# Performance work log

Measured on AMD Instinct MI355X. Metric: run time of the kernel, lower is better.

The kernel has to match this reference:

```python
import jax, jax.numpy as jnp
import numpy as np

BETA = 0.9       # leak factor (snn.Leaky beta)
THRESH = 1.0     # default snn.Leaky threshold
ALPHA = 2.0      # default ATan surrogate alpha

@jax.custom_vjp
def atan_spike(x):
    # Heaviside forward, ATan surrogate backward (snntorch default spike_grad)
    return (x > 0).astype(x.dtype)

def _atan_fwd(x):
    return (x > 0).astype(x.dtype), x

def _atan_bwd(x, g):
    # d/dx ~ (alpha/2) / (1 + (pi/2 * alpha * x)^2)
    return (g * (ALPHA / 2) / (1 + (jnp.pi / 2 * ALPHA * x) ** 2),)

atan_spike.defvjp(_atan_fwd, _atan_bwd)

def setup_inputs() -> dict:
    key = jax.random.key(0)
    k1, k2 = jax.random.split(key)
    B, IN, OUT, T = 64, 1024, 1024, 256
    x = jax.random.normal(k1, (B, IN, T), dtype=jnp.float32)
    W = jax.random.normal(k2, (OUT, IN), dtype=jnp.float32) * (1.0 / np.sqrt(IN))
    return {"x": x, "W": W}

def reference(x, W):
    # Batch all per-timestep GEMMs into one contraction: syn[b,o,t]
    syn = jnp.einsum('bit,oi->bot', x, W)
    syn_t = jnp.moveaxis(syn, -1, 0)  # [T, B, OUT]
    mem0 = jnp.zeros(syn.shape[:-1], syn.dtype)  # [B, OUT]

    def step(mem, s):
        # snntorch Leaky (subtract reset): reset from previous mem (detached),
        # then state update, then spike from new mem.
        reset = jax.lax.stop_gradient((mem > THRESH).astype(mem.dtype))
        mem = BETA * mem + s - reset * THRESH
        spk = atan_spike(mem - THRESH)
        return mem, spk

    _, spks = jax.lax.scan(step, mem0, syn_t)  # spks: [T, B, OUT]
    return jnp.moveaxis(spks, 0, -1)  # [B, OUT, T]
```

## Files before the change

kernel.cpp:

```cpp
#include <hip/hip_runtime.h>


#define B_DIM 64
#define IN_DIM 1024
#define OUT_DIM 1024
#define T_DIM 256

typedef int v4i __attribute__((ext_vector_type(4)));
typedef int v16i __attribute__((ext_vector_type(16)));
typedef double v4d __attribute__((ext_vector_type(4)));

#define LO_OFF   0ull
#define WSL_OFF  67108864ull
#define XSL_OFF  73400320ull
#define AL_OFF   174063616ull
#define BE_OFF   174067712ull
#define PART_OFF 174133248ull
#define WS_NEED  175181824ull

__device__ __forceinline__ void gload_lds16(const void* g, void* l)
{
    __builtin_amdgcn_global_load_lds(
        (const __attribute__((address_space(1))) void*)g,
        (__attribute__((address_space(3))) void*)l, 16, 0, 0);
}

__device__ __forceinline__ void dig4_extract(unsigned bits, int bem,
                                             signed char* d )
{
    const int be = (bits >> 23) & 255;
    unsigned M = (bits & 0x7fffffu) | (be ? 0x800000u : 0u);
    const int sh = be - bem + 4;
    unsigned fix = 0;
    if (sh >= 0) fix = M << sh;
    else if (sh > -32) fix = M >> (-sh);
    int d0 = (fix >> 21) & 127, d1 = (fix >> 14) & 127,
        d2 = (fix >> 7) & 127,  d3 = fix & 127;
    if (bits & 0x80000000u) { d0 = -d0; d1 = -d1; d2 = -d2; d3 = -d3; }
    d[0] = (signed char)d0; d[1] = (signed char)d1;
    d[2] = (signed char)d2; d[3] = (signed char)d3;
}

__global__ __launch_bounds__(256) void k_beta_part(const float* __restrict__ x,
                                                   float* __restrict__ part)
{
    const int ic = blockIdx.x;
    const int b  = blockIdx.y;
    const int t  = threadIdx.x;
    const float* p = x + ((size_t)b * IN_DIM + ic * 64) * T_DIM + t;
    float m = 0.f;
    #pragma unroll 4
    for (int i = 0; i < 64; ++i) m = fmaxf(m, fabsf(p[(size_t)i * T_DIM]));
    part[((size_t)b * 16 + ic) * T_DIM + t] = m;
}

__global__ __launch_bounds__(256) void k_beta(const float* __restrict__ part,
                                              int* __restrict__ beta_e)
{
    const int b = blockIdx.x, t = threadIdx.x;
    float m = 0.f;
    #pragma unroll
    for (int ic = 0; ic < 16; ++ic)
        m = fmaxf(m, part[((size_t)b * 16 + ic) * T_DIM + t]);
    int e = 0;
    if (m > 0.f) frexpf(m, &e);
    beta_e[b * T_DIM + t] = e;
}

__global__ __launch_bounds__(256) void k_slice_x(const float* __restrict__ x,
    const int* __restrict__ beta_e, signed char* __restrict__ xsl)
{
    __shared__ float ft[64][65];
    const int tb = blockIdx.x;
    const int ib = blockIdx.y;
    const int b  = blockIdx.z;
    const int tid = threadIdx.x;
    const int t0 = tb * 64, i0 = ib * 64;
    #pragma unroll
    for (int p = 0; p < 16; ++p) {
        int id = tid + p * 256;
        int il = id >> 6, tl = id & 63;
        ft[il][tl] = x[((size_t)b * IN_DIM + i0 + il) * T_DIM + t0 + tl];
    }
    __syncthreads();

    const int t32l = tid >> 7;
    const int ksl  = (tid >> 6) & 1;
    const int lane = tid & 63;
    const int t_local = t32l * 32 + (lane & 31);
    const int k_local = ksl * 32 + (lane >> 5) * 16;
    const int e = beta_e[b * T_DIM + t0 + t_local];
    const int bem = e + 126;

    signed char dig[16][4];
    #pragma unroll
    for (int j = 0; j < 16; ++j)
        dig4_extract(__float_as_uint(ft[k_local + j][t_local]), bem, dig[j]);

    #pragma unroll
    for (int p = 0; p < 4; ++p) {
        int w[4];
        #pragma unroll
        for (int g = 0; g < 4; ++g)
            w[g] = (dig[4*g][p] & 0xff) | ((dig[4*g+1][p] & 0xff) << 8) |
                   ((dig[4*g+2][p] & 0xff) << 16) | ((dig[4*g+3][p] & 0xff) << 24);
        const size_t base =
            ((((size_t)p * B_DIM + b) * 8 + (tb * 2 + t32l)) * 32 + (ib * 2 + ksl)) * 1024
            + lane * 16;
        *(v4i*)&xsl[base] = (v4i){w[0], w[1], w[2], w[3]};
    }
}

__global__ __launch_bounds__(256) void k_slice_w(const float* __restrict__ W,
    signed char* __restrict__ wsl, int* __restrict__ alpha_e)
{
    __shared__ float red[256];
    __shared__ float wrow[1024];
    __shared__ int se;
    const int o = blockIdx.x, tid = threadIdx.x;
    float4 v = *(const float4*)&W[(size_t)o * IN_DIM + tid * 4];
    *(float4*)&wrow[tid * 4] = v;
    float m = fmaxf(fmaxf(fabsf(v.x), fabsf(v.y)), fmaxf(fabsf(v.z), fabsf(v.w)));
    red[tid] = m; __syncthreads();
    for (int s = 128; s > 0; s >>= 1) {
        if (tid < s) red[tid] = fmaxf(red[tid], red[tid + s]);
        __syncthreads();
    }
    if (tid == 0) { int e = 0; if (red[0] > 0.f) frexpf(red[0], &e); se = e; alpha_e[o] = e; }
    __syncthreads();
    if (tid >= 64) return;
    const int bem = se + 126;
    const int ks = tid >> 1, khalf = tid & 1;
    const int k0 = tid * 16;
    const int lane = (o & 31) + 32 * khalf;

    signed char dig[16][4];
    #pragma unroll
    for (int j = 0; j < 16; ++j)
        dig4_extract(__float_as_uint(wrow[k0 + j]), bem, dig[j]);

    #pragma unroll
    for (int p = 0; p < 4; ++p) {
        int w[4];
        #pragma unroll
        for (int g = 0; g < 4; ++g)
            w[g] = (dig[4*g][p] & 0xff) | ((dig[4*g+1][p] & 0xff) << 8) |
                   ((dig[4*g+2][p] & 0xff) << 16) | ((dig[4*g+3][p] & 0xff) << 24);
        const size_t base =
            (((size_t)p * 32 + (o >> 5)) * 32 + ks) * 1024 + lane * 16;
        *(v4i*)&wsl[base] = (v4i){w[0], w[1], w[2], w[3]};
    }
}

#define OZ_LOADS(PF)                                                        \
    {                                                                       \
        _Pragma("unroll")                                                   \
        for (int j = 0; j < 4; ++j) {                                       \
            gload_lds16(gp[j], &LB[PF][lbase + j * 8192]);                  \
            gp[j] += 1024;                                                  \
        }                                                                   \
    }

#define OZ_MATH(CUR)                                                        \
    {                                                                       \
        const signed char* base_ = LB[CUR];                                 \
        v4i af[4];                                                          \
        _Pragma("unroll")                                                   \
        for (int p = 0; p < 4; ++p)                                         \
            af[p] = *(const v4i*)(base_ + p * 4096 + aoffm);                \
        __builtin_amdgcn_s_setprio(1);                                      \
        _Pragma("unroll")                                                   \
        for (int q = 0; q < 4; ++q) {                                       \
            v4i b0 = *(const v4i*)(base_ + 16384 + q * 4096 + boffm);       \
            v4i b1 = *(const v4i*)(base_ + 16384 + q * 4096 + boffm + 1024);\
            _Pragma("unroll")                                               \
            for (int p = 0; p + q < 4; ++p) {                               \
                accA[p + q] = __builtin_amdgcn_mfma_i32_32x32x32_i8(        \
                    af[p], b0, accA[p + q], 0, 0, 0);                       \
                accB[p + q] = __builtin_amdgcn_mfma_i32_32x32x32_i8(        \
                    af[p], b1, accB[p + q], 0, 0, 0);                       \
            }                                                               \
        }                                                                   \
        __builtin_amdgcn_s_setprio(0);                                      \
    }

#define VMBAR(N)                                                            \
    do {                                                                    \
        asm volatile("s_waitcnt vmcnt(" #N ")" ::: "memory");               \
        __builtin_amdgcn_s_barrier();                                       \
    } while (0)

__global__ __launch_bounds__(512, 2) void k_oz_gemm(
    const signed char* __restrict__ wsl, const signed char* __restrict__ xsl,
    const int* __restrict__ alpha_e, const int* __restrict__ beta_e,
    float* __restrict__ syn_hi, float* __restrict__ syn_lo)
{
    __shared__ __align__(16) signed char LB[3][32768];

    const int tid = threadIdx.x;
    const int lane = tid & 63, wave = tid >> 6;
    const int tb = blockIdx.x;
    const int ob = blockIdx.y;
    const int b  = blockIdx.z;
    const int o0 = ob * 128, t0 = tb * 128;
    const int woh = wave >> 1;
    const int wth = wave & 1;
    const int l16 = lane * 16;

    v16i accA[4], accB[4];
    #pragma unroll
    for (int s = 0; s < 4; ++s) {
        accA[s] = (v16i){0,0,0,0,0,0,0,0,0,0,0,0,0,0,0,0};
        accB[s] = (v16i){0,0,0,0,0,0,0,0,0,0,0,0,0,0,0,0};
    }

    const signed char* gp[4];
    #pragma unroll
    for (int j = 0; j < 4; ++j) {
        const int s = 8 * j + wave;
        if (s < 16) {
            gp[j] = wsl + ((size_t)(s >> 2) << 20)
                        + ((size_t)(4 * ob + (s & 3)) << 15) + l16;
        } else {
            const int t = s - 16;
            gp[j] = xsl + ((size_t)(t >> 2) << 24) + ((size_t)b << 18)
                        + ((size_t)(4 * tb + (t & 3)) << 15) + l16;
        }
    }
    const int lbase = wave * 1024;

    const int aoffm = woh * 1024 + l16;
    const int boffm = wth * 2048 + l16;

    OZ_LOADS(0)
    OZ_LOADS(1)
    VMBAR(4);

    #pragma unroll 1
    for (int it = 0; it < 10; ++it) {
        OZ_LOADS(2) OZ_MATH(0) VMBAR(4);
        OZ_LOADS(0) OZ_MATH(1) VMBAR(4);
        OZ_LOADS(1) OZ_MATH(2) VMBAR(4);
    }
    OZ_MATH(0) VMBAR(0);
    OZ_MATH(1)

    const int lr = lane & 31;
    const int rv = (lr + 1) * 0x01010101;
    const v4i pav  = {rv, rv, rv, rv};
    const v4i onev = {0x01010101, 0x01010101, 0x01010101, 0x01010101};
    const v16i z = (v16i){0,0,0,0,0,0,0,0,0,0,0,0,0,0,0,0};
    v16i d1 = __builtin_amdgcn_mfma_i32_32x32x32_i8(pav, onev, z, 0, 0, 0);
    v16i d2 = __builtin_amdgcn_mfma_i32_32x32x32_i8(onev, pav, z, 0, 0, 0);

    const int col = (d2[0] >> 5) - 1;
    const int gtA = t0 + wth * 64 + col;
    const int gtB = gtA + 32;
    const int ebA = beta_e[b * T_DIM + gtA];
    const int ebB = beta_e[b * T_DIM + gtB];
    float* ohiA = syn_hi + ((size_t)b * OUT_DIM + o0) * T_DIM + gtA;
    float* oloA = syn_lo + ((size_t)b * OUT_DIM + o0) * T_DIM + gtA;

    const double C0 = 0x1p-14, C1 = 0x1p-21, C2 = 0x1p-28, C3 = 0x1p-35;
    #pragma unroll
    for (int r = 0; r < 16; ++r) {
        const int row = (d1[r] >> 5) - 1;
        const int go = woh * 32 + row;
        const int ea = alpha_e[o0 + go];
        double vA = (double)accA[0][r] * C0 + (double)accA[1][r] * C1 +
                    (double)accA[2][r] * C2 + (double)accA[3][r] * C3;
        double vB = (double)accB[0][r] * C0 + (double)accB[1][r] * C1 +
                    (double)accB[2][r] * C2 + (double)accB[3][r] * C3;
        double synA = ldexp(vA, ea + ebA);
        double synB = ldexp(vB, ea + ebB);
        float hiA = (float)synA;
        float loA = (float)(synA - (double)hiA);
        float hiB = (float)synB;
        float loB = (float)(synB - (double)hiB);
        const size_t off = (size_t)go * T_DIM;
        ohiA[off] = hiA;       oloA[off] = loA;
        ohiA[off + 32] = hiB;  oloA[off + 32] = loB;
    }
}

#define BM 128
#define BN 128
#define BK 16
#define LDA 130

__global__ __launch_bounds__(256, 2) void spk_gemm_mfma64p_kernel(
    const float* __restrict__ x, const float* __restrict__ W,
    float* __restrict__ syn_hi, float* __restrict__ syn_lo)
{
    const int tid  = threadIdx.x;
    const int lane = tid & 63;
    const int wave = tid >> 6;
    const int tb = blockIdx.x, ob = blockIdx.y, b = blockIdx.z;

    __shared__ __align__(16) double As[BK][LDA];
    __shared__ __align__(16) double Bs[BK][LDA];

    const v4d zz = {0.0, 0.0, 0.0, 0.0};
    v4d d1 = __builtin_amdgcn_mfma_f64_16x16x4f64((double)lane, 1.0, zz, 0, 0, 0);
    v4d d2 = __builtin_amdgcn_mfma_f64_16x16x4f64(1.0, (double)lane, zz, 0, 0, 0);
    const bool a_h1 = (((int)d1[0] & 3) == 0);
    const bool b_h1 = (((int)d2[0] & 3) == 0);
    int drow[4];
    #pragma unroll
    for (int r = 0; r < 4; ++r) {
        const int v = (int)d1[r];
        drow[r] = (a_h1 ? (v - 96) >> 2 : (v - 6) >> 4) & 15;
    }
    const int am = a_h1 ? (lane & 15) : (lane >> 2);
    const int ak = a_h1 ? (lane >> 4) : (lane & 3);
    const int bn = b_h1 ? (lane & 15) : (lane >> 2);
    const int bk = b_h1 ? (lane >> 4) : (lane & 3);
    const int dcol = lane & 15;

    const int o0 = ob * BM, t0 = tb * BN;
    const float* Wp = W + (size_t)o0 * IN_DIM;
    const float* xp = x + (size_t)b * IN_DIM * T_DIM + t0;
    const int wo = (wave >> 1) * 64, wt = (wave & 1) * 64;

    v4d acc[4][4];
    #pragma unroll
    for (int i = 0; i < 4; ++i)
        #pragma unroll
        for (int j = 0; j < 4; ++j) acc[i][j] = zz;

    const int ar0 = tid / 4, ac = (tid % 4) * 4;
    const int bkr0 = tid / 32, btc = (tid % 32) * 4;

    float4 pa[2], pb[2];
    #pragma unroll
    for (int p = 0; p < 2; ++p) {
        pa[p] = *(const float4*)&Wp[(size_t)(ar0 + p * 64) * IN_DIM + ac];
        pb[p] = *(const float4*)&xp[(size_t)(bkr0 + p * 8) * T_DIM + btc];
    }

    for (int k0 = 0; k0 < IN_DIM; k0 += BK) {
        #pragma unroll
        for (int p = 0; p < 2; ++p) {
            const int r = ar0 + p * 64;
            As[ac + 0][r] = (double)pa[p].x; As[ac + 1][r] = (double)pa[p].y;
            As[ac + 2][r] = (double)pa[p].z; As[ac + 3][r] = (double)pa[p].w;
            const int kr = bkr0 + p * 8;
            Bs[kr][btc + 0] = (double)pb[p].x; Bs[kr][btc + 1] = (double)pb[p].y;
            Bs[kr][btc + 2] = (double)pb[p].z; Bs[kr][btc + 3] = (double)pb[p].w;
        }
        if (k0 + BK < IN_DIM) {
            #pragma unroll
            for (int p = 0; p < 2; ++p) {
                pa[p] = *(const float4*)&Wp[(size_t)(ar0 + p * 64) * IN_DIM + k0 + BK + ac];
                pb[p] = *(const float4*)&xp[(size_t)(bkr0 + p * 8 + k0 + BK) * T_DIM + btc];
            }
        }
        __syncthreads();
        #pragma unroll
        for (int kk = 0; kk < 4; ++kk) {
            const int kra = kk * 4 + ak, krb = kk * 4 + bk;
            double a[4], bb[4];
            #pragma unroll
            for (int i = 0; i < 4; ++i) a[i] = As[kra][wo + i * 16 + am];
            #pragma unroll
            for (int j = 0; j < 4; ++j) bb[j] = Bs[krb][wt + j * 16 + bn];
            #pragma unroll
            for (int i = 0; i < 4; ++i)
                #pragma unroll
                for (int j = 0; j < 4; ++j)
                    acc[i][j] = __builtin_amdgcn_mfma_f64_16x16x4f64(a[i], bb[j], acc[i][j], 0, 0, 0);
        }
        __syncthreads();
    }

    float* ohi = syn_hi + ((size_t)b * OUT_DIM + o0) * T_DIM + t0;
    float* olo = syn_lo + ((size_t)b * OUT_DIM + o0) * T_DIM + t0;
    #pragma unroll
    for (int i = 0; i < 4; ++i)
        #pragma unroll
        for (int j = 0; j < 4; ++j) {
            const int col = wt + j * 16 + dcol;
            #pragma unroll
            for (int r = 0; r < 4; ++r) {
                double s = acc[i][j][r];
                float hi = (float)s;
                float lo = (float)(s - (double)hi);
                const size_t off = (size_t)(wo + i * 16 + drow[r]) * T_DIM + col;
                ohi[off] = hi; olo[off] = lo;
            }
        }
}

__global__ __launch_bounds__(256) void spk_scan_f64_kernel(
    float* __restrict__ hi, const float* __restrict__ lo)
{
    const int TC = 16;
    __shared__ float thi[256][TC + 1];
    __shared__ float tlo[256][TC + 1];
    const int tid = threadIdx.x;
    const size_t row0 = (size_t)blockIdx.x * 256;

    double mem = 0.0;
    for (int t0 = 0; t0 < T_DIM; t0 += TC) {
        #pragma unroll
        for (int p = 0; p < 4; ++p) {
            int id = tid + p * 256;
            int r = id / 4, c = (id % 4) * 4;
            size_t g = (row0 + r) * T_DIM + t0 + c;
            float4 vh = *(const float4*)&hi[g];
            thi[r][c] = vh.x; thi[r][c+1] = vh.y; thi[r][c+2] = vh.z; thi[r][c+3] = vh.w;
            float4 vl = *(const float4*)&lo[g];
            tlo[r][c] = vl.x; tlo[r][c+1] = vl.y; tlo[r][c+2] = vl.z; tlo[r][c+3] = vl.w;
        }
        __syncthreads();
        float spk[TC];
        #pragma unroll
        for (int t = 0; t < TC; ++t) {
            double s = (double)thi[tid][t] + (double)tlo[tid][t];
            double reset = (mem > 1.0) ? 1.0 : 0.0;
            mem = 0.9 * mem + s - reset;
            spk[t] = ((mem - 1.0) > 0.0) ? 1.0f : 0.0f;
        }
        __syncthreads();
        #pragma unroll
        for (int t = 0; t < TC; ++t) thi[tid][t] = spk[t];
        __syncthreads();
        #pragma unroll
        for (int p = 0; p < 4; ++p) {
            int id = tid + p * 256;
            int r = id / 4, c = (id % 4) * 4;
            float4 v = make_float4(thi[r][c], thi[r][c+1], thi[r][c+2], thi[r][c+3]);
            *(float4*)&hi[(row0 + r) * T_DIM + t0 + c] = v;
        }
        __syncthreads();
    }
}

extern "C" void kernel_launch(void* const* d_in, const int* in_sizes, int n_in,
                              void* d_out, int out_size, void* d_ws, size_t ws_size,
                              hipStream_t stream)
{
    const float* x = (const float*)d_in[0];
    const float* W = (const float*)d_in[1];
    float* hi = (float*)d_out;
    char* ws = (char*)d_ws;
    float* lo = (float*)(ws + LO_OFF);

    if (ws_size >= WS_NEED) {
        signed char* wsl = (signed char*)(ws + WSL_OFF);
        signed char* xsl = (signed char*)(ws + XSL_OFF);
        int* alpha = (int*)(ws + AL_OFF);
        int* beta  = (int*)(ws + BE_OFF);
        float* part = (float*)(ws + PART_OFF);

        k_beta_part<<<dim3(16, B_DIM), dim3(256), 0, stream>>>(x, part);
        k_beta<<<dim3(B_DIM), dim3(256), 0, stream>>>(part, beta);
        k_slice_w<<<dim3(OUT_DIM), dim3(256), 0, stream>>>(W, wsl, alpha);
        k_slice_x<<<dim3(4, 16, B_DIM), dim3(256), 0, stream>>>(x, beta, xsl);
        k_oz_gemm<<<dim3(2, 8, B_DIM), dim3(512), 0, stream>>>(wsl, xsl, alpha, beta, hi, lo);
    } else {
        spk_gemm_mfma64p_kernel<<<dim3(2, 8, B_DIM), dim3(256), 0, stream>>>(x, W, hi, lo);
    }
    spk_scan_f64_kernel<<<dim3((B_DIM * OUT_DIM) / 256), dim3(256), 0, stream>>>(hi, lo);
}
```

Measured before the change: 348.4 us.

## Fuse LIF scan into Ozaki int8 GEMM epilogue with full-T tiles

The int8 sliced GEMM is retiled so each block covers 64 outputs by all 256 timesteps instead of 128x128. This lets the block run the membrane recurrence itself from an LDS staging buffer and write spikes directly. The fusion removes the hi/lo float intermediate written to global memory and the separate scan kernel launch. In exchange, the scan runs serially on a single wave per 64-step chunk while the other waves sit idle. LDS use grows to 120 KB per block, which may reduce occupancy.

```diff
diff --git a/kernel.cpp b/kernel.cpp
--- a/kernel.cpp
+++ b/kernel.cpp
@@ -155,7 +155,7 @@
 #define OZ_LOADS(PF)                                                        \
     {                                                                       \
         _Pragma("unroll")                                                   \
-        for (int j = 0; j < 4; ++j) {                                       \
+        for (int j = 0; j < 5; ++j) {                                       \
             gload_lds16(gp[j], &LB[PF][lbase + j * 8192]);                  \
             gp[j] += 1024;                                                  \
         }                                                                   \
@@ -167,12 +167,12 @@
         v4i af[4];                                                          \
         _Pragma("unroll")                                                   \
         for (int p = 0; p < 4; ++p)                                         \
-            af[p] = *(const v4i*)(base_ + p * 4096 + aoffm);                \
+            af[p] = *(const v4i*)(base_ + p * 2048 + aoffm);                \
         __builtin_amdgcn_s_setprio(1);                                      \
         _Pragma("unroll")                                                   \
         for (int q = 0; q < 4; ++q) {                                       \
-            v4i b0 = *(const v4i*)(base_ + 16384 + q * 4096 + boffm);       \
-            v4i b1 = *(const v4i*)(base_ + 16384 + q * 4096 + boffm + 1024);\
+            v4i b0 = *(const v4i*)(base_ + q * 8192 + boffm);               \
+            v4i b1 = *(const v4i*)(base_ + q * 8192 + boffm + 1024);        \
             _Pragma("unroll")                                               \
             for (int p = 0; p + q < 4; ++p) {                               \
                 accA[p + q] = __builtin_amdgcn_mfma_i32_32x32x32_i8(        \
@@ -190,21 +190,20 @@
         __builtin_amdgcn_s_barrier();                                       \
     } while (0)
 
-__global__ __launch_bounds__(512, 2) void k_oz_gemm(
+__global__ __launch_bounds__(512, 2) void k_oz_gemm_fused(
     const signed char* __restrict__ wsl, const signed char* __restrict__ xsl,
     const int* __restrict__ alpha_e, const int* __restrict__ beta_e,
-    float* __restrict__ syn_hi, float* __restrict__ syn_lo)
-{
-    __shared__ __align__(16) signed char LB[3][32768];
+    float* __restrict__ out)
+{
+    __shared__ __align__(16) signed char LB[3][40960];
 
     const int tid = threadIdx.x;
     const int lane = tid & 63, wave = tid >> 6;
-    const int tb = blockIdx.x;
-    const int ob = blockIdx.y;
-    const int b  = blockIdx.z;
-    const int o0 = ob * 128, t0 = tb * 128;
-    const int woh = wave >> 1;
-    const int wth = wave & 1;
+    const int ob = blockIdx.x;
+    const int b  = blockIdx.y;
+    const int o0 = ob * 64;
+    const int woh = wave >> 2;
+    const int wtq = wave & 3;
     const int l16 = lane * 16;
 
     v16i accA[4], accB[4];
@@ -214,33 +213,33 @@
         accB[s] = (v16i){0,0,0,0,0,0,0,0,0,0,0,0,0,0,0,0};
     }
 
-    const signed char* gp[4];
-    #pragma unroll
-    for (int j = 0; j < 4; ++j) {
+    const signed char* gp[5];
+    #pragma unroll
+    for (int j = 0; j < 5; ++j) {
         const int s = 8 * j + wave;
-        if (s < 16) {
-            gp[j] = wsl + ((size_t)(s >> 2) << 20)
-                        + ((size_t)(4 * ob + (s & 3)) << 15) + l16;
+        if (s < 8) {
+            gp[j] = wsl + ((size_t)(s >> 1) << 20)
+                        + ((size_t)(2 * ob + (s & 1)) << 15) + l16;
         } else {
-            const int t = s - 16;
-            gp[j] = xsl + ((size_t)(t >> 2) << 24) + ((size_t)b << 18)
-                        + ((size_t)(4 * tb + (t & 3)) << 15) + l16;
+            const int u = s - 8;
+            gp[j] = xsl + ((size_t)(u >> 3) << 24) + ((size_t)b << 18)
+                        + ((size_t)(u & 7) << 15) + l16;
         }
     }
     const int lbase = wave * 1024;
 
     const int aoffm = woh * 1024 + l16;
-    const int boffm = wth * 2048 + l16;
+    const int boffm = 8192 + wtq * 2048 + l16;
 
     OZ_LOADS(0)
     OZ_LOADS(1)
-    VMBAR(4);
+    VMBAR(5);
 
     #pragma unroll 1
     for (int it = 0; it < 10; ++it) {
-        OZ_LOADS(2) OZ_MATH(0) VMBAR(4);
-        OZ_LOADS(0) OZ_MATH(1) VMBAR(4);
-        OZ_LOADS(1) OZ_MATH(2) VMBAR(4);
+        OZ_LOADS(2) OZ_MATH(0) VMBAR(5);
+        OZ_LOADS(0) OZ_MATH(1) VMBAR(5);
+        OZ_LOADS(1) OZ_MATH(2) VMBAR(5);
     }
     OZ_MATH(0) VMBAR(0);
     OZ_MATH(1)
@@ -254,32 +253,63 @@
     v16i d2 = __builtin_amdgcn_mfma_i32_32x32x32_i8(onev, pav, z, 0, 0, 0);
 
     const int col = (d2[0] >> 5) - 1;
-    const int gtA = t0 + wth * 64 + col;
+    const int gtA = wtq * 64 + col;
     const int gtB = gtA + 32;
     const int ebA = beta_e[b * T_DIM + gtA];
     const int ebB = beta_e[b * T_DIM + gtB];
-    float* ohiA = syn_hi + ((size_t)b * OUT_DIM + o0) * T_DIM + gtA;
-    float* oloA = syn_lo + ((size_t)b * OUT_DIM + o0) * T_DIM + gtA;
 
     const double C0 = 0x1p-14, C1 = 0x1p-21, C2 = 0x1p-28, C3 = 0x1p-35;
+    double synA_[16], synB_[16];
+    int go_[16];
     #pragma unroll
     for (int r = 0; r < 16; ++r) {
         const int row = (d1[r] >> 5) - 1;
         const int go = woh * 32 + row;
+        go_[r] = go;
         const int ea = alpha_e[o0 + go];
         double vA = (double)accA[0][r] * C0 + (double)accA[1][r] * C1 +
                     (double)accA[2][r] * C2 + (double)accA[3][r] * C3;
         double vB = (double)accB[0][r] * C0 + (double)accB[1][r] * C1 +
                     (double)accB[2][r] * C2 + (double)accB[3][r] * C3;
-        double synA = ldexp(vA, ea + ebA);
-        double synB = ldexp(vB, ea + ebB);
-        float hiA = (float)synA;
-        float loA = (float)(synA - (double)hiA);
-        float hiB = (float)synB;
-        float loB = (float)(synB - (double)hiB);
-        const size_t off = (size_t)go * T_DIM;
-        ohiA[off] = hiA;       oloA[off] = loA;
-        ohiA[off + 32] = hiB;  oloA[off + 32] = loB;
+        synA_[r] = ldexp(vA, ea + ebA);
+        synB_[r] = ldexp(vB, ea + ebB);
+    }
+
+    double* synbuf = (double*)&LB[0][0];
+    float*  spkbuf = (float*)&LB[1][0];
+    float*  outp = out + ((size_t)b * OUT_DIM + o0) * T_DIM;
+    double mem = 0.0;
+
+    __syncthreads();
+    #pragma unroll 1
+    for (int c = 0; c < 4; ++c) {
+        if (wtq == c) {
+            #pragma unroll
+            for (int r = 0; r < 16; ++r) {
+                synbuf[(size_t)col * 65 + go_[r]]        = synA_[r];
+                synbuf[(size_t)(col + 32) * 65 + go_[r]] = synB_[r];
+            }
+        }
+        __syncthreads();
+        if (wave == 0) {
+            #pragma unroll 8
+            for (int tt = 0; tt < 64; ++tt) {
+                double s = synbuf[(size_t)tt * 65 + lane];
+                double reset = (mem > 1.0) ? 1.0 : 0.0;
+                mem = 0.9 * mem + s - reset;
+                spkbuf[lane * 68 + tt] = ((mem - 1.0) > 0.0) ? 1.0f : 0.0f;
+            }
+        }
+        __syncthreads();
+        {
+            const int o = tid >> 3, tg = tid & 7;
+            float4 v0 = *(float4*)&spkbuf[o * 68 + tg * 8];
+            float4 v1 = *(float4*)&spkbuf[o * 68 + tg * 8 + 4];
+            float* dst = outp + (size_t)o * T_DIM + c * 64 + tg * 8;
+            *(float4*)&dst[0] = v0;
+            *(float4*)&dst[4] = v1;
+        }
+        __syncthreads();
     }
 }
 
@@ -457,9 +487,9 @@
         k_beta<<<dim3(B_DIM), dim3(256), 0, stream>>>(part, beta);
         k_slice_w<<<dim3(OUT_DIM), dim3(256), 0, stream>>>(W, wsl, alpha);
         k_slice_x<<<dim3(4, 16, B_DIM), dim3(256), 0, stream>>>(x, beta, xsl);
-        k_oz_gemm<<<dim3(2, 8, B_DIM), dim3(512), 0, stream>>>(wsl, xsl, alpha, beta, hi, lo);
+        k_oz_gemm_fused<<<dim3(16, B_DIM), dim3(512), 0, stream>>>(wsl, xsl, alpha, beta, hi);
     } else {
         spk_gemm_mfma64p_kernel<<<dim3(2, 8, B_DIM), dim3(256), 0, stream>>>(x, W, hi, lo);
-    }
-    spk_scan_f64_kernel<<<dim3((B_DIM * OUT_DIM) / 256), dim3(256), 0, stream>>>(hi, lo);
-}
+        spk_scan_f64_kernel<<<dim3((B_DIM * OUT_DIM) / 256), dim3(256), 0, stream>>>(hi, lo);
+    }
+}
```

Result: no change. 346.4 us (-0.5%).
